# Performance work log

Measured on AMD Instinct MI355X. Metric: run time of the kernel, lower is better.

The kernel has to match this reference:

```python
import jax, jax.numpy as jnp
import numpy as np

NEG_SLOPE = 0.01  # torch LeakyReLU default

N_NODES = 100000
H_C = 128
N_EDGES = 1600000


def setup_inputs() -> dict:
    key = jax.random.key(0)
    k1, k2, k3, k4, k5, k6 = jax.random.split(key, 6)
    z = jax.random.normal(k1, (N_NODES, H_C), dtype=jnp.float32)
    edge_label_index = jax.random.randint(k2, (2, N_EDGES), 0, N_NODES, dtype=jnp.int64)
    # torch Linear: weight [out, in], bias [out]
    W1 = jax.random.normal(k3, (H_C, 2 * H_C), dtype=jnp.float32) / np.sqrt(2 * H_C)
    b1 = jax.random.normal(k4, (H_C,), dtype=jnp.float32) * 0.01
    W2 = jax.random.normal(k5, (1, H_C), dtype=jnp.float32) / np.sqrt(H_C)
    b2 = jax.random.normal(k6, (1,), dtype=jnp.float32) * 0.01
    return {"z": z, "edge_label_index": edge_label_index,
            "W1": W1, "b1": b1, "W2": W2, "b2": b2}


def reference(z, edge_label_index, W1, b1, W2, b2):
    row, col = edge_label_index[0], edge_label_index[1]
    # cat([z[row], z[col]], dim=1) @ W1.T == z[row] @ W1[:, :H].T + z[col] @ W1[:, H:].T
    h = z.shape[1]
    W1a, W1b = W1[:, :h], W1[:, h:]
    zc = jnp.einsum('eh,oh->eo', z[row], W1a) + jnp.einsum('eh,oh->eo', z[col], W1b) + b1
    zc = jnp.where(zc >= 0, zc, NEG_SLOPE * zc)  # LeakyReLU
    out = jnp.einsum('eh,oh->eo', zc, W2) + b2   # [E, 1]
    return out.reshape(-1)
```

## Files before the change

### kernel.cpp

```cpp
#include <hip/hip_runtime.h>
#include <hip/hip_fp16.h>

#define NN 100000
#define HC 128
#define NE 1600000

typedef float f32x4 __attribute__((ext_vector_type(4)));
typedef short bf16x8 __attribute__((ext_vector_type(8)));

__device__ __forceinline__ unsigned short f2bf(float f) {
  union { float f; unsigned u; } c; c.f = f;
  unsigned u = c.u + (0x7FFFu + ((c.u >> 16) & 1u));
  return (unsigned short)(u >> 16);
}
__device__ __forceinline__ float bf2f(unsigned short b) {
  union { unsigned u; float f; } c; c.u = ((unsigned)b) << 16;
  return c.f;
}

__global__ __launch_bounds__(256) void wprep2_kernel(
    const float* __restrict__ W1, unsigned short* __restrict__ Whf,
    unsigned short* __restrict__ Wlf) {
  const int f = blockIdx.x * 256 + threadIdx.x;
  if (f >= 4096) return;
  const int lane = f & 63;
  const int kg = (f >> 6) & 3;
  const int ot = f >> 8;
  const int lr = lane & 15;
  const int lg = lane >> 4;
  const int o = ot * 16 + lr;
  const int kb = kg * 32 + lg * 8;
  const float* __restrict__ src =
      W1 + (size_t)(o & 127) * 256 + ((o >> 7) << 7) + kb;
#pragma unroll
  for (int e = 0; e < 8; ++e) {
    const float v = src[e];
    const unsigned short hi = f2bf(v);
    Whf[(size_t)f * 8 + e] = hi;
    Wlf[(size_t)f * 8 + e] = f2bf(v - bf2f(hi));
  }
}

__global__ __launch_bounds__(256) void precompute_uv_mfma5_kernel(
    const float* __restrict__ z, const unsigned short* __restrict__ Whf,
    const unsigned short* __restrict__ Wlf, __half* __restrict__ UV) {
  __shared__ char zs[32 * 512];

  const int t = threadIdx.x;
  const int lane = t & 63;
  const int wv = t >> 6;
  const int nb = blockIdx.x * 32;
  const int lr = lane & 15;
  const int lg = lane >> 4;

#pragma unroll
  for (int i = 0; i < 4; ++i) {
    const int ci = t + 256 * i;
    const int row = ci >> 5;
    const int c16 = ci & 31;
    const float4 v = *(const float4*)(z + (size_t)(nb + row) * HC + c16 * 4);
    const int dst = (row * 512 + c16 * 16) ^ ((row & 7) << 4);
    *(float4*)(zs + dst) = v;
  }
  __syncthreads();

  bf16x8 bh[2][4], bl[2][4];
#pragma unroll
  for (int ms = 0; ms < 2; ++ms) {
    const int row = ms * 16 + lr;
    const int sw = (row & 7) << 4;
#pragma unroll
    for (int kg = 0; kg < 4; ++kg) {
      const int c16 = kg * 8 + lg * 2;
      const float4 p0 = *(const float4*)(zs + ((row * 512 + c16 * 16) ^ sw));
      const float4 p1 = *(const float4*)(zs + ((row * 512 + (c16 + 1) * 16) ^ sw));
      const float v[8] = {p0.x, p0.y, p0.z, p0.w, p1.x, p1.y, p1.z, p1.w};
#pragma unroll
      for (int e = 0; e < 8; ++e) {
        const unsigned short hi = f2bf(v[e]);
        bh[ms][kg][e] = (short)hi;
        bl[ms][kg][e] = (short)f2bf(v[e] - bf2f(hi));
      }
    }
  }

#pragma unroll 1
  for (int nt = 0; nt < 4; ++nt) {
    const int ot = wv * 4 + nt;
    const unsigned short* __restrict__ wph = Whf + ((size_t)(ot * 4) * 64 + lane) * 8;
    const unsigned short* __restrict__ wpl = Wlf + ((size_t)(ot * 4) * 64 + lane) * 8;

    f32x4 acc0 = {0.f, 0.f, 0.f, 0.f};
    f32x4 acc1 = {0.f, 0.f, 0.f, 0.f};
#pragma unroll
    for (int kg = 0; kg < 4; ++kg) {
      const bf16x8 ah = *(const bf16x8*)(wph + (size_t)kg * 64 * 8);
      const bf16x8 al = *(const bf16x8*)(wpl + (size_t)kg * 64 * 8);
      acc0 = __builtin_amdgcn_mfma_f32_16x16x32_bf16(ah, bh[0][kg], acc0, 0, 0, 0);
      acc0 = __builtin_amdgcn_mfma_f32_16x16x32_bf16(al, bh[0][kg], acc0, 0, 0, 0);
      acc0 = __builtin_amdgcn_mfma_f32_16x16x32_bf16(ah, bl[0][kg], acc0, 0, 0, 0);
      acc1 = __builtin_amdgcn_mfma_f32_16x16x32_bf16(ah, bh[1][kg], acc1, 0, 0, 0);
      acc1 = __builtin_amdgcn_mfma_f32_16x16x32_bf16(al, bh[1][kg], acc1, 0, 0, 0);
      acc1 = __builtin_amdgcn_mfma_f32_16x16x32_bf16(ah, bl[1][kg], acc1, 0, 0, 0);
    }

    const int ob = ot * 16 + lg * 4;
    {
      const int node = nb + lr;
      union { uint2 u; __half2 h[2]; } pk;
      pk.h[0] = __floats2half2_rn(acc0[0], acc0[1]);
      pk.h[1] = __floats2half2_rn(acc0[2], acc0[3]);
      *(uint2*)(UV + (size_t)node * 256 + ob) = pk.u;
    }
    {
      const int node = nb + 16 + lr;
      union { uint2 u; __half2 h[2]; } pk;
      pk.h[0] = __floats2half2_rn(acc1[0], acc1[1]);
      pk.h[1] = __floats2half2_rn(acc1[2], acc1[3]);
      *(uint2*)(UV + (size_t)node * 256 + ob) = pk.u;
    }
  }
}

__global__ __launch_bounds__(256) void edge_decode_f16_kernel(
    const int* __restrict__ eidx, const __half* __restrict__ UV,
    const float* __restrict__ b1, const float* __restrict__ W2,
    const float* __restrict__ b2, float* __restrict__ out,
    int e0, int e1) {
  const int lane = threadIdx.x & 15;
  const int qw = (blockIdx.x * 256 + threadIdx.x) >> 4;
  const int nqw = (gridDim.x * 256) >> 4;

  const float4 b1a = ((const float4*)b1)[2 * lane];
  const float4 b1b = ((const float4*)b1)[2 * lane + 1];
  const float4 w2a = ((const float4*)W2)[2 * lane];
  const float4 w2b = ((const float4*)W2)[2 * lane + 1];
  const float bb[8] = {b1a.x, b1a.y, b1a.z, b1a.w, b1b.x, b1b.y, b1b.z, b1b.w};
  const float ww[8] = {w2a.x, w2a.y, w2a.z, w2a.w, w2b.x, w2b.y, w2b.z, w2b.w};
  const float bias2 = b2[0];

  const int* __restrict__ rows = eidx;
  const int* __restrict__ cols = eidx + NE;

#pragma unroll 2
  for (int e = e0 + qw; e < e1; e += nqw) {
    const int r = rows[e];
    const int c = cols[e];
    union { uint4 u; __half2 h[4]; } Uu, Vv;
    Uu.u = *(const uint4*)(UV + (size_t)r * 256 + lane * 8);
    Vv.u = *(const uint4*)(UV + (size_t)c * 256 + 128 + lane * 8);

    float s = 0.f;
#pragma unroll
    for (int k = 0; k < 4; ++k) {
      const float2 uf = __half22float2(Uu.h[k]);
      const float2 vf = __half22float2(Vv.h[k]);
      float t0 = uf.x + vf.x + bb[2 * k];
      t0 = (t0 >= 0.f) ? t0 : 0.01f * t0;
      s = fmaf(t0, ww[2 * k], s);
      float t1 = uf.y + vf.y + bb[2 * k + 1];
      t1 = (t1 >= 0.f) ? t1 : 0.01f * t1;
      s = fmaf(t1, ww[2 * k + 1], s);
    }

    s += __shfl_xor(s, 8);
    s += __shfl_xor(s, 4);
    s += __shfl_xor(s, 2);
    s += __shfl_xor(s, 1);
    if (lane == 0) out[e] = s + bias2;
  }
}

__global__ __launch_bounds__(64) void edge_direct_kernel(
    const float* __restrict__ z, const int* __restrict__ eidx,
    const float* __restrict__ W1, const float* __restrict__ b1,
    const float* __restrict__ W2, const float* __restrict__ b2,
    float* __restrict__ out) {
  const int lane = threadIdx.x;
  const int o0 = lane, o1 = lane + 64;
  const float w2_0 = W2[o0], w2_1 = W2[o1];
  const float b1_0 = b1[o0], b1_1 = b1[o1];
  const float bias2 = b2[0];

  for (int e = blockIdx.x; e < NE; e += gridDim.x) {
    const int r = eidx[e];
    const int c = eidx[e + NE];
    const float* __restrict__ zr = z + (size_t)r * HC;
    const float* __restrict__ zc = z + (size_t)c * HC;
    float a0 = 0.f, a1 = 0.f;
    for (int h = 0; h < HC; ++h) {
      const float zrh = zr[h], zch = zc[h];
      a0 = fmaf(zrh, W1[(size_t)o0 * 256 + h], a0);
      a0 = fmaf(zch, W1[(size_t)o0 * 256 + 128 + h], a0);
      a1 = fmaf(zrh, W1[(size_t)o1 * 256 + h], a1);
      a1 = fmaf(zch, W1[(size_t)o1 * 256 + 128 + h], a1);
    }
    a0 += b1_0; a1 += b1_1;
    a0 = (a0 >= 0.f) ? a0 : 0.01f * a0;
    a1 = (a1 >= 0.f) ? a1 : 0.01f * a1;
    float s = fmaf(a0, w2_0, a1 * w2_1);
    for (int off = 32; off >= 1; off >>= 1) s += __shfl_xor(s, off);
    if (lane == 0) out[e] = s + bias2;
  }
}

extern "C" void kernel_launch(void* const* d_in, const int* in_sizes, int n_in,
                              void* d_out, int out_size, void* d_ws, size_t ws_size,
                              hipStream_t stream) {
  const float* z  = (const float*)d_in[0];
  const int*   ei = (const int*)d_in[1];
  const float* W1 = (const float*)d_in[2];
  const float* b1 = (const float*)d_in[3];
  const float* W2 = (const float*)d_in[4];
  const float* b2 = (const float*)d_in[5];
  float* out = (float*)d_out;

  const size_t uv_bytes = (size_t)NN * 256 * sizeof(__half);
  const size_t w_bytes  = (size_t)256 * 128 * sizeof(unsigned short);

  if (ws_size >= uv_bytes + 2 * w_bytes) {
    __half* UV = (__half*)d_ws;
    unsigned short* Whf = (unsigned short*)((char*)d_ws + uv_bytes);
    unsigned short* Wlf = Whf + 256 * 128;
    wprep2_kernel<<<16, 256, 0, stream>>>(W1, Whf, Wlf);
    precompute_uv_mfma5_kernel<<<NN / 32, 256, 0, stream>>>(z, Whf, Wlf, UV);
    for (int q = 0; q < 4; ++q) {
      edge_decode_f16_kernel<<<2048, 256, 0, stream>>>(
          ei, UV, b1, W2, b2, out, q * (NE / 4), (q + 1) * (NE / 4));
    }
  } else {
    edge_direct_kernel<<<8192, 64, 0, stream>>>(z, ei, W1, b1, W2, b2, out);
  }
}
```

Before: 162.1 us.

## Double-buffer z tiles in UV precompute to overlap loads with MFMA

Each block of the UV precompute kernel now handles two 32-node tiles with two LDS buffers. The second tile's global-to-LDS staging is issued before the first tile's MFMA compute and store, so the load latency can hide behind compute. The grid is halved and LDS use per block doubles, which may lower occupancy. A guard skips the second tile when the node count is not a multiple of 64.

Result: slower. 168.3 us (+3.8%).

```diff
diff --git a/kernel.cpp b/kernel.cpp
--- a/kernel.cpp
+++ b/kernel.cpp
@@ -41,84 +41,105 @@
   }
 }
 
-__global__ __launch_bounds__(256) void precompute_uv_mfma5_kernel(
+__global__ __launch_bounds__(256) void precompute_uv_mfma7_kernel(
     const float* __restrict__ z, const unsigned short* __restrict__ Whf,
     const unsigned short* __restrict__ Wlf, __half* __restrict__ UV) {
-  __shared__ char zs[32 * 512];
+  __shared__ char zs[2][16384];
 
   const int t = threadIdx.x;
   const int lane = t & 63;
   const int wv = t >> 6;
-  const int nb = blockIdx.x * 32;
   const int lr = lane & 15;
   const int lg = lane >> 4;
-
-#pragma unroll
-  for (int i = 0; i < 4; ++i) {
-    const int ci = t + 256 * i;
-    const int row = ci >> 5;
-    const int c16 = ci & 31;
-    const float4 v = *(const float4*)(z + (size_t)(nb + row) * HC + c16 * 4);
-    const int dst = (row * 512 + c16 * 16) ^ ((row & 7) << 4);
-    *(float4*)(zs + dst) = v;
-  }
+  const int nb0 = blockIdx.x * 64;
+  const int nb1 = nb0 + 32;
+  const bool has2 = (nb1 < NN);
+
+  bf16x8 bh[2][4], bl[2][4];
+
+  auto stage = [&](char* buf, int nb) {
+#pragma unroll
+    for (int i = 0; i < 4; ++i) {
+      const int ci = t + 256 * i;
+      const int row = ci >> 5;
+      const int c16 = ci & 31;
+      const float4 v = *(const float4*)(z + (size_t)(nb + row) * HC + c16 * 4);
+      const int dst = (row * 512 + c16 * 16) ^ ((row & 7) << 4);
+      *(float4*)(buf + dst) = v;
+    }
+  };
+
+  auto read_frags = [&](const char* buf) {
+#pragma unroll
+    for (int ms = 0; ms < 2; ++ms) {
+      const int row = ms * 16 + lr;
+      const int sw = (row & 7) << 4;
+#pragma unroll
+      for (int kg = 0; kg < 4; ++kg) {
+        const int c16 = kg * 8 + lg * 2;
+        const float4 p0 = *(const float4*)(buf + ((row * 512 + c16 * 16) ^ sw));
+        const float4 p1 = *(const float4*)(buf + ((row * 512 + (c16 + 1) * 16) ^ sw));
+        const float v[8] = {p0.x, p0.y, p0.z, p0.w, p1.x, p1.y, p1.z, p1.w};
+#pragma unroll
+        for (int e = 0; e < 8; ++e) {
+          const unsigned short hi = f2bf(v[e]);
+          bh[ms][kg][e] = (short)hi;
+          bl[ms][kg][e] = (short)f2bf(v[e] - bf2f(hi));
+        }
+      }
+    }
+  };
+
+  auto compute_store = [&](int nb) {
+#pragma unroll 1
+    for (int nt = 0; nt < 4; ++nt) {
+      const int ot = wv * 4 + nt;
+      const unsigned short* __restrict__ wph =
+          Whf + ((size_t)(ot * 4) * 64 + lane) * 8;
+      const unsigned short* __restrict__ wpl =
+          Wlf + ((size_t)(ot * 4) * 64 + lane) * 8;
+
+      f32x4 acc0 = {0.f, 0.f, 0.f, 0.f};
+      f32x4 acc1 = {0.f, 0.f, 0.f, 0.f};
+#pragma unroll
+      for (int kg = 0; kg < 4; ++kg) {
+        const bf16x8 ah = *(const bf16x8*)(wph + (size_t)kg * 64 * 8);
+        const bf16x8 al = *(const bf16x8*)(wpl + (size_t)kg * 64 * 8);
+        acc0 = __builtin_amdgcn_mfma_f32_16x16x32_bf16(ah, bh[0][kg], acc0, 0, 0, 0);
+        acc0 = __builtin_amdgcn_mfma_f32_16x16x32_bf16(al, bh[0][kg], acc0, 0, 0, 0);
+        acc0 = __builtin_amdgcn_mfma_f32_16x16x32_bf16(ah, bl[0][kg], acc0, 0, 0, 0);
+        acc1 = __builtin_amdgcn_mfma_f32_16x16x32_bf16(ah, bh[1][kg], acc1, 0, 0, 0);
+        acc1 = __builtin_amdgcn_mfma_f32_16x16x32_bf16(al, bh[1][kg], acc1, 0, 0, 0);
+        acc1 = __builtin_amdgcn_mfma_f32_16x16x32_bf16(ah, bl[1][kg], acc1, 0, 0, 0);
+      }
+
+      const int ob = ot * 16 + lg * 4;
+      {
+        const int node = nb + lr;
+        union { uint2 u; __half2 h[2]; } pk;
+        pk.h[0] = __floats2half2_rn(acc0[0], acc0[1]);
+        pk.h[1] = __floats2half2_rn(acc0[2], acc0[3]);
+        *(uint2*)(UV + (size_t)node * 256 + ob) = pk.u;
+      }
+      {
+        const int node = nb + 16 + lr;
+        union { uint2 u; __half2 h[2]; } pk;
+        pk.h[0] = __floats2half2_rn(acc1[0], acc1[1]);
+        pk.h[1] = __floats2half2_rn(acc1[2], acc1[3]);
+        *(uint2*)(UV + (size_t)node * 256 + ob) = pk.u;
+      }
+    }
+  };
+
+  stage(zs[0], nb0);
   __syncthreads();
-
-  bf16x8 bh[2][4], bl[2][4];
-#pragma unroll
-  for (int ms = 0; ms < 2; ++ms) {
-    const int row = ms * 16 + lr;
-    const int sw = (row & 7) << 4;
-#pragma unroll
-    for (int kg = 0; kg < 4; ++kg) {
-      const int c16 = kg * 8 + lg * 2;
-      const float4 p0 = *(const float4*)(zs + ((row * 512 + c16 * 16) ^ sw));
-      const float4 p1 = *(const float4*)(zs + ((row * 512 + (c16 + 1) * 16) ^ sw));
-      const float v[8] = {p0.x, p0.y, p0.z, p0.w, p1.x, p1.y, p1.z, p1.w};
-#pragma unroll
-      for (int e = 0; e < 8; ++e) {
-        const unsigned short hi = f2bf(v[e]);
-        bh[ms][kg][e] = (short)hi;
-        bl[ms][kg][e] = (short)f2bf(v[e] - bf2f(hi));
-      }
-    }
-  }
-
-#pragma unroll 1
-  for (int nt = 0; nt < 4; ++nt) {
-    const int ot = wv * 4 + nt;
-    const unsigned short* __restrict__ wph = Whf + ((size_t)(ot * 4) * 64 + lane) * 8;
-    const unsigned short* __restrict__ wpl = Wlf + ((size_t)(ot * 4) * 64 + lane) * 8;
-
-    f32x4 acc0 = {0.f, 0.f, 0.f, 0.f};
-    f32x4 acc1 = {0.f, 0.f, 0.f, 0.f};
-#pragma unroll
-    for (int kg = 0; kg < 4; ++kg) {
-      const bf16x8 ah = *(const bf16x8*)(wph + (size_t)kg * 64 * 8);
-      const bf16x8 al = *(const bf16x8*)(wpl + (size_t)kg * 64 * 8);
-      acc0 = __builtin_amdgcn_mfma_f32_16x16x32_bf16(ah, bh[0][kg], acc0, 0, 0, 0);
-      acc0 = __builtin_amdgcn_mfma_f32_16x16x32_bf16(al, bh[0][kg], acc0, 0, 0, 0);
-      acc0 = __builtin_amdgcn_mfma_f32_16x16x32_bf16(ah, bl[0][kg], acc0, 0, 0, 0);
-      acc1 = __builtin_amdgcn_mfma_f32_16x16x32_bf16(ah, bh[1][kg], acc1, 0, 0, 0);
-      acc1 = __builtin_amdgcn_mfma_f32_16x16x32_bf16(al, bh[1][kg], acc1, 0, 0, 0);
-      acc1 = __builtin_amdgcn_mfma_f32_16x16x32_bf16(ah, bl[1][kg], acc1, 0, 0, 0);
-    }
-
-    const int ob = ot * 16 + lg * 4;
-    {
-      const int node = nb + lr;
-      union { uint2 u; __half2 h[2]; } pk;
-      pk.h[0] = __floats2half2_rn(acc0[0], acc0[1]);
-      pk.h[1] = __floats2half2_rn(acc0[2], acc0[3]);
-      *(uint2*)(UV + (size_t)node * 256 + ob) = pk.u;
-    }
-    {
-      const int node = nb + 16 + lr;
-      union { uint2 u; __half2 h[2]; } pk;
-      pk.h[0] = __floats2half2_rn(acc1[0], acc1[1]);
-      pk.h[1] = __floats2half2_rn(acc1[2], acc1[3]);
-      *(uint2*)(UV + (size_t)node * 256 + ob) = pk.u;
-    }
+  read_frags(zs[0]);
+  if (has2) stage(zs[1], nb1);
+  compute_store(nb0);
+  __syncthreads();
+  if (has2) {
+    read_frags(zs[1]);
+    compute_store(nb1);
   }
 }
 
@@ -223,7 +244,7 @@
     unsigned short* Whf = (unsigned short*)((char*)d_ws + uv_bytes);
     unsigned short* Wlf = Whf + 256 * 128;
     wprep2_kernel<<<16, 256, 0, stream>>>(W1, Whf, Wlf);
-    precompute_uv_mfma5_kernel<<<NN / 32, 256, 0, stream>>>(z, Whf, Wlf, UV);
+    precompute_uv_mfma7_kernel<<<(NN + 63) / 64, 256, 0, stream>>>(z, Whf, Wlf, UV);
     for (int q = 0; q < 4; ++q) {
       edge_decode_f16_kernel<<<2048, 256, 0, stream>>>(
           ei, UV, b1, W2, b2, out, q * (NE / 4), (q + 1) * (NE / 4));
```
